# Kernel optimization log

Hardware: AMD Instinct MI355X
Metric: run time of the kernel (lower is better)

## Reference

```python
import jax, jax.numpy as jnp
import numpy as np

N = 50000      # nodes
E = 800000     # edges (avg degree 16)
DIM = 256      # in_channels == heads * out_channels
H = 8          # heads
C = DIM // H   # per-head out_channels = 32
EDGE_DIM = 2
NEG_SLOPE = 0.2


def setup_inputs() -> dict:
    key = jax.random.key(0)
    ks = jax.random.split(key, 8)
    x = jax.random.normal(ks[0], (N, DIM), dtype=jnp.float32)
    edge_index = jax.random.randint(ks[1], (2, E), 0, N, dtype=jnp.int32)
    edge_attr = jax.random.normal(ks[2], (E, EDGE_DIM), dtype=jnp.float32)
    s = 1.0 / np.sqrt(DIM)
    W_l = jax.random.normal(ks[3], (DIM, H * C), dtype=jnp.float32) * s   # lin_l (src)
    W_r = jax.random.normal(ks[4], (DIM, H * C), dtype=jnp.float32) * s   # lin_r (dst)
    W_e = jax.random.normal(ks[5], (EDGE_DIM, H * C), dtype=jnp.float32) * (1.0 / np.sqrt(EDGE_DIM))
    att = jax.random.normal(ks[6], (H, C), dtype=jnp.float32) * s         # attention vector a
    bias = jnp.zeros((H * C,), dtype=jnp.float32)
    return {"x": x, "edge_index": edge_index, "edge_attr": edge_attr,
            "W_l": W_l, "W_r": W_r, "W_e": W_e, "att": att, "bias": bias}


def reference(x, edge_index, edge_attr, W_l, W_r, W_e, att, bias):
    src, dst = edge_index[0], edge_index[1]
    # --- add self loops; fill_value='mean' => scatter-mean of incoming edge_attr per node ---
    attr_sum = jax.ops.segment_sum(edge_attr, dst, num_segments=N)          # [N, 2]
    cnt = jax.ops.segment_sum(jnp.ones((edge_attr.shape[0], 1), edge_attr.dtype), dst, num_segments=N)
    loop_attr = attr_sum / jnp.maximum(cnt, 1.0)                             # [N, 2], 0 for isolated nodes
    idx = jnp.arange(N, dtype=src.dtype)
    src_a = jnp.concatenate([src, idx])                                      # [E+N]
    dst_a = jnp.concatenate([dst, idx])
    ea = jnp.concatenate([edge_attr, loop_attr], axis=0)                     # [E+N, 2]
    # --- GATv2: project src/dst/edge features ---
    x_l = (x @ W_l).reshape(N, H, C)
    x_r = (x @ W_r).reshape(N, H, C)
    e_e = (ea @ W_e).reshape(-1, H, C)                                       # [E+N, H, C]
    m = x_l[src_a] + x_r[dst_a] + e_e                                        # [E+N, H, C]
    score = jnp.einsum('ehc,hc->eh', jax.nn.leaky_relu(m, NEG_SLOPE), att)   # [E+N, H]
    # --- segment softmax over incoming edges of each dst (self loop guarantees >=1 edge) ---
    smax = jax.ops.segment_max(score, dst_a, num_segments=N)                 # [N, H]
    ex = jnp.exp(score - smax[dst_a])
    denom = jax.ops.segment_sum(ex, dst_a, num_segments=N)                   # [N, H]
    alpha = ex / denom[dst_a]                                                # [E+N, H]
    # --- weighted scatter-add of src messages ---
    out = jax.ops.segment_sum(alpha[..., None] * x_l[src_a], dst_a, num_segments=N)  # [N, H, C]
    return out.reshape(N, H * C) + bias
```

## Files before the change

kernel.cpp:

```cpp
#include <hip/hip_runtime.h>
#include <hip/hip_bf16.h>

#define NN 50000
#define NPAD 53248
#define EE 800000
#define DIM 256
#define NEG_SLOPE 0.2f
#define LOG2E 1.44269504088896f

#define GEMM_BLOCKS 1564
#define FILL_BLOCKS 3125
#define MIX_BLOCKS  15625
#define WT_BLOCKS   512

typedef __attribute__((ext_vector_type(8))) short short8;
typedef __attribute__((ext_vector_type(4))) float f32x4;
typedef __attribute__((ext_vector_type(2))) float v2f;

__device__ __forceinline__ unsigned short f2bf(float f) {
    unsigned u = __float_as_uint(f);
    unsigned r = (u + 0x7fffu + ((u >> 16) & 1u)) >> 16;
    return (unsigned short)r;
}
__device__ __forceinline__ float u2f_lo(unsigned u) {
    return __uint_as_float(u << 16);
}
__device__ __forceinline__ float u2f_hi(unsigned u) {
    return __uint_as_float(u & 0xffff0000u);
}

__device__ __forceinline__ float red8(float s) {
    int t;
    t = __builtin_amdgcn_update_dpp(0, __float_as_int(s), 0xB1, 0xF, 0xF, true);
    s += __int_as_float(t);
    t = __builtin_amdgcn_update_dpp(0, __float_as_int(s), 0x4E, 0xF, 0xF, true);
    s += __int_as_float(t);
    t = __builtin_amdgcn_update_dpp(0, __float_as_int(s), 0x141, 0xF, 0xF, true);
    s += __int_as_float(t);
    return s;
}

__global__ __launch_bounds__(256) void k_prep_count(
    const float* __restrict__ x, const float* __restrict__ Wl,
    const float* __restrict__ Wr, const int* __restrict__ ei,
    unsigned short* __restrict__ xb, unsigned short* __restrict__ wt,
    int* __restrict__ cnt, int* __restrict__ rank)
{
    int b = blockIdx.x;
    if (b < MIX_BLOCKS) {
        int g = b / 5;
        if (b - g * 5 == 0) {
            int e = g * 256 + threadIdx.x;
            int dst = ei[EE + e];
            rank[e] = atomicAdd(&cnt[dst], 1);
        } else {
            int ci = b - g - 1;
            int i = (ci * 256 + threadIdx.x) * 4;
            float4 v = *(const float4*)(x + i);
            ushort4 o;
            o.x = f2bf(v.x); o.y = f2bf(v.y); o.z = f2bf(v.z); o.w = f2bf(v.w);
            *(ushort4*)(xb + i) = o;
        }
    } else {
        int idx = (b - MIX_BLOCKS) * 256 + threadIdx.x;
        int n = idx >> 8, k = idx & 255;
        float v = (n < 256) ? Wl[k * 256 + n] : Wr[k * 256 + (n - 256)];
        wt[idx] = f2bf(v);
    }
}

__global__ __launch_bounds__(1024) void k_scan(
    const int* __restrict__ cnt, int* __restrict__ row_start)
{
    __shared__ int wsum[16];
    int tid = threadIdx.x, lane = tid & 63, wid = tid >> 6;
    int4 v[13];
#pragma unroll
    for (int p = 0; p < 13; ++p)
        v[p] = *(const int4*)(cnt + p * 4096 + tid * 4);
    int carry = 0;
#pragma unroll
    for (int p = 0; p < 13; ++p) {
        int4 vv = v[p];
        int tsum = vv.x + vv.y + vv.z + vv.w;
        int s = tsum;
#pragma unroll
        for (int off = 1; off < 64; off <<= 1) {
            int t = __shfl_up(s, off, 64);
            if (lane >= off) s += t;
        }
        if (lane == 63) wsum[wid] = s;
        __syncthreads();
        int wpre = 0, tot = 0;
#pragma unroll
        for (int w = 0; w < 16; ++w) {
            int xv = wsum[w];
            tot += xv;
            if (w < wid) wpre += xv;
        }
        int ex = carry + wpre + (s - tsum);
        int4 o;
        o.x = ex;
        o.y = o.x + vv.x;
        o.z = o.y + vv.y;
        o.w = o.z + vv.z;
        *(int4*)(row_start + p * 4096 + tid * 4) = o;
        carry += tot;
        __syncthreads();
    }
}

__global__ __launch_bounds__(256) void k_gemm_fill(
    const unsigned short* __restrict__ xb, const unsigned short* __restrict__ wt,
    const int* __restrict__ ei, const float* __restrict__ ea,
    const int* __restrict__ row_start, const int* __restrict__ rank,
    unsigned short* __restrict__ xl, unsigned short* __restrict__ xr,
    uint2* __restrict__ edge_rec)
{
    __shared__ short sAB[8192];
    int tid = threadIdx.x;

    if (blockIdx.x >= GEMM_BLOCKS) {
        int e = (blockIdx.x - GEMM_BLOCKS) * 256 + tid;
        if (e < EE) {
            int src = ei[e];
            int dst = ei[EE + e];
            float2 a = *(const float2*)(ea + 2 * e);
            int pos = row_start[dst] + rank[e];
            unsigned packed = ((unsigned)f2bf(a.y) << 16) | f2bf(a.x);
            edge_rec[pos] = make_uint2((unsigned)src, packed);
        }
        return;
    }

    int bid = blockIdx.x;
    const int q = GEMM_BLOCKS / 8, r = GEMM_BLOCKS % 8;
    int xcd = bid & 7, kk = bid >> 3;
    int wg = (xcd < r) ? xcd * (q + 1) + kk
                       : r * (q + 1) + (xcd - r) * q + kk;

    int wid = tid >> 6, lane = tid & 63;
    int mt = wg >> 2, nt = wg & 3;
    int mBase = mt * 128, nBase = nt * 128;
    int wm = (wid & 1) * 64, wn = (wid >> 1) * 64;
    int qq4 = lane >> 4, mh = lane & 15;

    f32x4 acc[4][4];
#pragma unroll
    for (int i = 0; i < 4; ++i)
#pragma unroll
        for (int j = 0; j < 4; ++j)
            acc[i][j] = (f32x4){0.f, 0.f, 0.f, 0.f};

    int aoff[4], boff[4];
#pragma unroll
    for (int f = 0; f < 4; ++f) {
        int rr = wm + f * 16 + mh;
        aoff[f] = (rr * 4 + (qq4 ^ (rr & 3))) * 8;
        int nl = wn + f * 16 + mh;
        boff[f] = 4096 + (nl * 4 + (qq4 ^ (nl & 3))) * 8;
    }

    for (int k0 = 0; k0 < 256; k0 += 32) {
        __syncthreads();
#pragma unroll
        for (int it = 0; it < 4; ++it) {
            int L = it * 256 + tid;
            const unsigned short* g;
            if (L < 512) {
                int rr = L >> 2;
                int q2 = (L & 3) ^ (rr & 3);
                int grow = mBase + rr;
                if (grow > NN - 1) grow = NN - 1;
                g = xb + (size_t)grow * 256 + k0 + q2 * 8;
            } else {
                int LB = L - 512;
                int nl = LB >> 2;
                int q2 = (LB & 3) ^ (nl & 3);
                g = wt + (size_t)(nBase + nl) * 256 + k0 + q2 * 8;
            }
            short* lp = sAB + (it * 256 + wid * 64) * 8;
            __builtin_amdgcn_global_load_lds(
                (const __attribute__((address_space(1))) void*)g,
                (__attribute__((address_space(3))) void*)lp, 16, 0, 0);
        }
        __syncthreads();

        short8 af[4], bfr[4];
#pragma unroll
        for (int f = 0; f < 4; ++f) af[f]  = *(const short8*)(sAB + aoff[f]);
#pragma unroll
        for (int f = 0; f < 4; ++f) bfr[f] = *(const short8*)(sAB + boff[f]);
#pragma unroll
        for (int i = 0; i < 4; ++i)
#pragma unroll
            for (int j = 0; j < 4; ++j)
                acc[i][j] = __builtin_amdgcn_mfma_f32_16x16x32_bf16(
                    af[i], bfr[j], acc[i][j], 0, 0, 0);
    }

    unsigned short* cb = (nt < 2) ? xl : xr;
    int chalf = (nt & 1) * 128;
#pragma unroll
    for (int i = 0; i < 4; ++i)
#pragma unroll
        for (int j = 0; j < 4; ++j)
#pragma unroll
            for (int rr = 0; rr < 4; ++rr) {
                int row = mBase + wm + i * 16 + qq4 * 4 + rr;
                if (row < NN) {
                    int col = chalf + wn + j * 16 + mh;
                    cb[(size_t)row * 256 + col] = f2bf(acc[i][j][rr]);
                }
            }
}

__global__ __launch_bounds__(256) void k_attn(
    const unsigned short* __restrict__ xl, const unsigned short* __restrict__ xr,
    const int* __restrict__ row_start, const uint2* __restrict__ edge_rec,
    const float* __restrict__ W_e, const float* __restrict__ att,
    const float* __restrict__ bias, float* __restrict__ out)
{
    int n = __builtin_amdgcn_readfirstlane(blockIdx.x * 4 + (threadIdx.x >> 6));
    if (n >= NN) return;
    int lane = threadIdx.x & 63;
    int j = lane * 4;

    uint2 xru = *(const uint2*)(xr + ((size_t)n << 8) + j);
    v2f xr01 = {u2f_lo(xru.x), u2f_hi(xru.x)};
    v2f xr23 = {u2f_lo(xru.y), u2f_hi(xru.y)};
    float4 av = *(const float4*)(att + j);
    v2f att01 = {av.x * LOG2E, av.y * LOG2E};
    v2f att23 = {av.z * LOG2E, av.w * LOG2E};
    float4 w0v = *(const float4*)(W_e + j);
    float4 w1v = *(const float4*)(W_e + 256 + j);
    v2f we0_01 = {w0v.x, w0v.y}, we0_23 = {w0v.z, w0v.w};
    v2f we1_01 = {w1v.x, w1v.y}, we1_23 = {w1v.z, w1v.w};
    const v2f sl2 = {NEG_SLOPE, NEG_SLOPE};

    int rs = __builtin_amdgcn_readfirstlane(row_start[n]);
    int cn = __builtin_amdgcn_readfirstlane(row_start[n + 1]) - rs;

    float D = 0.0f, la0 = 0.0f, la1 = 0.0f;
    v2f acc01 = {0.f, 0.f}, acc23 = {0.f, 0.f};

    auto body = [&](uint2 ru, float a0, float a1) {
        v2f xl01 = {u2f_lo(ru.x), u2f_hi(ru.x)};
        v2f xl23 = {u2f_lo(ru.y), u2f_hi(ru.y)};
        v2f a0v = {a0, a0}, a1v = {a1, a1};
        v2f m01 = xl01 + xr01;
        v2f m23 = xl23 + xr23;
        m01 = __builtin_elementwise_fma(a0v, we0_01, m01);
        m23 = __builtin_elementwise_fma(a0v, we0_23, m23);
        m01 = __builtin_elementwise_fma(a1v, we1_01, m01);
        m23 = __builtin_elementwise_fma(a1v, we1_23, m23);
        v2f t01 = __builtin_elementwise_max(m01, m01 * sl2);
        v2f t23 = __builtin_elementwise_max(m23, m23 * sl2);
        v2f sv = t01 * att01;
        sv = __builtin_elementwise_fma(t23, att23, sv);
        float s = sv.x + sv.y;
        s = red8(s);
        float w = __builtin_amdgcn_exp2f(s);
        D += w;
        v2f wv = {w, w};
        acc01 = __builtin_elementwise_fma(wv, xl01, acc01);
        acc23 = __builtin_elementwise_fma(wv, xl23, acc23);
    };

    int done = 0;
    while (done < cn) {
        int m = cn - done; if (m > 64) m = 64;
        int ridx = rs + done + lane;
        if (ridx > EE + 63) ridx = EE + 63;
        uint2 rc = edge_rec[ridx];
        int rcx = (int)rc.x, rca = (int)rc.y;

        auto gat = [&](int k) -> uint2 {
            unsigned sidx = (unsigned)__builtin_amdgcn_readlane(rcx, k);
            return *(const uint2*)(xl + ((size_t)sidx << 8) + j);
        };
        auto proc = [&](uint2 xu, int k) {
            unsigned pk = (unsigned)__builtin_amdgcn_readlane(rca, k);
            float a0 = __uint_as_float(pk << 16);
            float a1 = __uint_as_float(pk & 0xffff0000u);
            la0 += a0; la1 += a1;
            body(xu, a0, a1);
        };

        uint2 x0 = gat(0), x1 = gat(1), x2 = gat(2), x3 = gat(3);
        uint2 x4 = gat(4), x5 = gat(5), x6 = gat(6), x7 = gat(7);
        for (int i = 0; i < m; i += 8) {
            proc(x0, i);
            if (i +  8 < m) x0 = gat(i +  8);
            if (i + 1 < m) { proc(x1, i + 1); if (i +  9 < m) x1 = gat(i +  9); }
            if (i + 2 < m) { proc(x2, i + 2); if (i + 10 < m) x2 = gat(i + 10); }
            if (i + 3 < m) { proc(x3, i + 3); if (i + 11 < m) x3 = gat(i + 11); }
            if (i + 4 < m) { proc(x4, i + 4); if (i + 12 < m) x4 = gat(i + 12); }
            if (i + 5 < m) { proc(x5, i + 5); if (i + 13 < m) x5 = gat(i + 13); }
            if (i + 6 < m) { proc(x6, i + 6); if (i + 14 < m) x6 = gat(i + 14); }
            if (i + 7 < m) { proc(x7, i + 7); if (i + 15 < m) x7 = gat(i + 15); }
        }
        done += m;
    }

    float invc = 1.0f / fmaxf((float)cn, 1.0f);
    uint2 xs = *(const uint2*)(xl + ((size_t)n << 8) + j);
    body(xs, la0 * invc, la1 * invc);

    float invD = 1.0f / D;
    float4 b4 = *(const float4*)(bias + j);
    float4 o;
    o.x = fmaf(acc01.x, invD, b4.x);
    o.y = fmaf(acc01.y, invD, b4.y);
    o.z = fmaf(acc23.x, invD, b4.z);
    o.w = fmaf(acc23.y, invD, b4.w);
    *(float4*)(out + (size_t)n * 256 + j) = o;
}

extern "C" void kernel_launch(void* const* d_in, const int* in_sizes, int n_in,
                              void* d_out, int out_size, void* d_ws, size_t ws_size,
                              hipStream_t stream)
{
    const float* x    = (const float*)d_in[0];
    const int*   ei   = (const int*)  d_in[1];
    const float* ea   = (const float*)d_in[2];
    const float* Wl   = (const float*)d_in[3];
    const float* Wr   = (const float*)d_in[4];
    const float* We   = (const float*)d_in[5];
    const float* att  = (const float*)d_in[6];
    const float* bias = (const float*)d_in[7];
    float* out = (float*)d_out;

    char* ws = (char*)d_ws;
    size_t off = 0;
    unsigned short* xl = (unsigned short*)(ws + off); off += (size_t)NN * 256 * 2;
    unsigned short* xr = (unsigned short*)(ws + off); off += (size_t)NN * 256 * 2;
    unsigned short* xb = (unsigned short*)(ws + off); off += (size_t)NN * 256 * 2;
    uint2*  edge_rec   = (uint2*)(ws + off);          off += (size_t)(EE + 64) * 8;
    int*    cnt        = (int*)(ws + off);            off += (size_t)NPAD * 4;
    int*    row_st     = (int*)(ws + off);            off += (size_t)NPAD * 4;
    int*    rank       = (int*)(ws + off);            off += (size_t)EE * 4;
    unsigned short* wt = (unsigned short*)(ws + off); off += (size_t)512 * 256 * 2;

    hipMemsetAsync(edge_rec + EE, 0, 64 * sizeof(uint2) + NPAD * sizeof(int), stream);

    k_prep_count<<<MIX_BLOCKS + WT_BLOCKS, 256, 0, stream>>>(
        x, Wl, Wr, ei, xb, wt, cnt, rank);
    k_scan      <<<1, 1024, 0, stream>>>(cnt, row_st);
    k_gemm_fill <<<GEMM_BLOCKS + FILL_BLOCKS, 256, 0, stream>>>(
        xb, wt, ei, ea, row_st, rank, xl, xr, edge_rec);
    k_attn      <<<12500, 256, 0, stream>>>(
        xl, xr, row_st, edge_rec, We, att, bias, out);
}
```

Baseline: 258.7 us.

## Partition degree-count atomics per XCD and store compact 16-bit ranks

Replaces the single global per-node counter with eight per-XCD counter arrays. Each edge does a workgroup-scope atomic on the array for its own XCC (read from a hardware register) and records a 16-bit rank that packs the XCD id with a local rank. A new pre-reduction kernel turns the per-XCD counts into exclusive offsets and writes per-node totals, which the existing scan then scans in place. The aim is to avoid contended device-scope atomics across XCDs and to halve the rank traffic. The cost is an extra kernel launch, a larger counter buffer to clear and read, and reliance on workgroup-scope atomics staying coherent within an XCD's L2.

```diff
diff --git a/kernel.cpp b/kernel.cpp
--- a/kernel.cpp
+++ b/kernel.cpp
@@ -7,11 +7,13 @@
 #define DIM 256
 #define NEG_SLOPE 0.2f
 #define LOG2E 1.44269504088896f
+#define CSTR 50048
 
 #define GEMM_BLOCKS 1564
 #define FILL_BLOCKS 3125
 #define MIX_BLOCKS  15625
 #define WT_BLOCKS   512
+#define PRERED_BLOCKS 208
 
 typedef __attribute__((ext_vector_type(8))) short short8;
 typedef __attribute__((ext_vector_type(4))) float f32x4;
@@ -44,7 +46,7 @@
     const float* __restrict__ x, const float* __restrict__ Wl,
     const float* __restrict__ Wr, const int* __restrict__ ei,
     unsigned short* __restrict__ xb, unsigned short* __restrict__ wt,
-    int* __restrict__ cnt, int* __restrict__ rank)
+    unsigned* __restrict__ cnt_x, unsigned short* __restrict__ rank16)
 {
     int b = blockIdx.x;
     if (b < MIX_BLOCKS) {
@@ -52,7 +54,13 @@
         if (b - g * 5 == 0) {
             int e = g * 256 + threadIdx.x;
             int dst = ei[EE + e];
-            rank[e] = atomicAdd(&cnt[dst], 1);
+            unsigned xcc;
+            asm volatile("s_getreg_b32 %0, hwreg(HW_REG_XCC_ID)" : "=s"(xcc));
+            xcc &= 7u;
+            unsigned rl = __hip_atomic_fetch_add(
+                &cnt_x[xcc * CSTR + (unsigned)dst], 1u,
+                __ATOMIC_RELAXED, __HIP_MEMORY_SCOPE_WORKGROUP);
+            rank16[e] = (unsigned short)((xcc << 8) | rl);
         } else {
             int ci = b - g - 1;
             int i = (ci * 256 + threadIdx.x) * 4;
@@ -69,15 +77,30 @@
     }
 }
 
-__global__ __launch_bounds__(1024) void k_scan(
-    const int* __restrict__ cnt, int* __restrict__ row_start)
+__global__ __launch_bounds__(256) void k_prered(
+    unsigned* __restrict__ cnt_x, int* __restrict__ row_st)
+{
+    int d = blockIdx.x * 256 + threadIdx.x;
+    unsigned s = 0;
+    if (d < CSTR) {
+#pragma unroll
+        for (int c = 0; c < 8; ++c) {
+            unsigned v = cnt_x[c * CSTR + d];
+            cnt_x[c * CSTR + d] = s;
+            s += v;
+        }
+    }
+    row_st[d] = (int)s;
+}
+
+__global__ __launch_bounds__(1024) void k_scan(int* __restrict__ a)
 {
     __shared__ int wsum[16];
     int tid = threadIdx.x, lane = tid & 63, wid = tid >> 6;
     int4 v[13];
 #pragma unroll
     for (int p = 0; p < 13; ++p)
-        v[p] = *(const int4*)(cnt + p * 4096 + tid * 4);
+        v[p] = *(const int4*)(a + p * 4096 + tid * 4);
     int carry = 0;
 #pragma unroll
     for (int p = 0; p < 13; ++p) {
@@ -104,7 +127,7 @@
         o.y = o.x + vv.x;
         o.z = o.y + vv.y;
         o.w = o.z + vv.z;
-        *(int4*)(row_start + p * 4096 + tid * 4) = o;
+        *(int4*)(a + p * 4096 + tid * 4) = o;
         carry += tot;
         __syncthreads();
     }
@@ -113,7 +136,8 @@
 __global__ __launch_bounds__(256) void k_gemm_fill(
     const unsigned short* __restrict__ xb, const unsigned short* __restrict__ wt,
     const int* __restrict__ ei, const float* __restrict__ ea,
-    const int* __restrict__ row_start, const int* __restrict__ rank,
+    const int* __restrict__ row_start, const unsigned short* __restrict__ rank16,
+    const unsigned* __restrict__ cnt_x,
     unsigned short* __restrict__ xl, unsigned short* __restrict__ xr,
     uint2* __restrict__ edge_rec)
 {
@@ -126,7 +150,9 @@
             int src = ei[e];
             int dst = ei[EE + e];
             float2 a = *(const float2*)(ea + 2 * e);
-            int pos = row_start[dst] + rank[e];
+            int rk = rank16[e];
+            int c = rk >> 8, rl = rk & 255;
+            int pos = row_start[dst] + (int)cnt_x[c * CSTR + dst] + rl;
             unsigned packed = ((unsigned)f2bf(a.y) << 16) | f2bf(a.x);
             edge_rec[pos] = make_uint2((unsigned)src, packed);
         }
@@ -337,18 +363,20 @@
     unsigned short* xr = (unsigned short*)(ws + off); off += (size_t)NN * 256 * 2;
     unsigned short* xb = (unsigned short*)(ws + off); off += (size_t)NN * 256 * 2;
     uint2*  edge_rec   = (uint2*)(ws + off);          off += (size_t)(EE + 64) * 8;
-    int*    cnt        = (int*)(ws + off);            off += (size_t)NPAD * 4;
+    unsigned* cnt_x    = (unsigned*)(ws + off);       off += (size_t)8 * CSTR * 4;
     int*    row_st     = (int*)(ws + off);            off += (size_t)NPAD * 4;
-    int*    rank       = (int*)(ws + off);            off += (size_t)EE * 4;
+    unsigned short* rank16 = (unsigned short*)(ws + off); off += (size_t)EE * 2;
     unsigned short* wt = (unsigned short*)(ws + off); off += (size_t)512 * 256 * 2;
 
-    hipMemsetAsync(edge_rec + EE, 0, 64 * sizeof(uint2) + NPAD * sizeof(int), stream);
+    hipMemsetAsync(edge_rec + EE, 0,
+                   64 * sizeof(uint2) + (size_t)8 * CSTR * 4, stream);
 
     k_prep_count<<<MIX_BLOCKS + WT_BLOCKS, 256, 0, stream>>>(
-        x, Wl, Wr, ei, xb, wt, cnt, rank);
-    k_scan      <<<1, 1024, 0, stream>>>(cnt, row_st);
+        x, Wl, Wr, ei, xb, wt, cnt_x, rank16);
+    k_prered    <<<PRERED_BLOCKS, 256, 0, stream>>>(cnt_x, row_st);
+    k_scan      <<<1, 1024, 0, stream>>>(row_st);
     k_gemm_fill <<<GEMM_BLOCKS + FILL_BLOCKS, 256, 0, stream>>>(
-        xb, wt, ei, ea, row_st, rank, xl, xr, edge_rec);
+        xb, wt, ei, ea, row_st, rank16, cnt_x, xl, xr, edge_rec);
     k_attn      <<<12500, 256, 0, stream>>>(
         xl, xr, row_st, edge_rec, We, att, bias, out);
 }
```

After: 262.7 us. Within noise of the previous version (+1.5%).

## Replace global-atomic CSR build with per-block LDS histograms and column scan

Applied to the files above, without the earlier changes.

Builds the destination-sorted edge list with per-block shared-memory histograms (16-bit packed counters) instead of global atomics per edge. A column scan over the block histograms and a global scan give each block a deterministic offset, and a fill kernel recomputes local ranks with LDS atomics. This removes the per-edge rank array and the contended global atomics. In exchange it adds more kernel launches, reuses the bf16 x buffer as histogram scratch after the GEMM, and serialises the GEMM with the CSR build instead of running them in one fused launch.

```diff
diff --git a/kernel.cpp b/kernel.cpp
--- a/kernel.cpp
+++ b/kernel.cpp
@@ -8,10 +8,14 @@
 #define NEG_SLOPE 0.2f
 #define LOG2E 1.44269504088896f
 
+#define CSTR 50000
+#define HIST_BLOCKS 256
+#define EPB 3125
+
 #define GEMM_BLOCKS 1564
-#define FILL_BLOCKS 3125
-#define MIX_BLOCKS  15625
+#define CVT_BLOCKS  12500
 #define WT_BLOCKS   512
+#define COLS_BLOCKS 208
 
 typedef __attribute__((ext_vector_type(8))) short short8;
 typedef __attribute__((ext_vector_type(4))) float f32x4;
@@ -40,98 +44,32 @@
     return s;
 }
 
-__global__ __launch_bounds__(256) void k_prep_count(
+__global__ __launch_bounds__(256) void k_prep(
     const float* __restrict__ x, const float* __restrict__ Wl,
-    const float* __restrict__ Wr, const int* __restrict__ ei,
-    unsigned short* __restrict__ xb, unsigned short* __restrict__ wt,
-    int* __restrict__ cnt, int* __restrict__ rank)
+    const float* __restrict__ Wr,
+    unsigned short* __restrict__ xb, unsigned short* __restrict__ wt)
 {
     int b = blockIdx.x;
-    if (b < MIX_BLOCKS) {
-        int g = b / 5;
-        if (b - g * 5 == 0) {
-            int e = g * 256 + threadIdx.x;
-            int dst = ei[EE + e];
-            rank[e] = atomicAdd(&cnt[dst], 1);
-        } else {
-            int ci = b - g - 1;
-            int i = (ci * 256 + threadIdx.x) * 4;
-            float4 v = *(const float4*)(x + i);
-            ushort4 o;
-            o.x = f2bf(v.x); o.y = f2bf(v.y); o.z = f2bf(v.z); o.w = f2bf(v.w);
-            *(ushort4*)(xb + i) = o;
-        }
+    if (b < CVT_BLOCKS) {
+        int i = (b * 256 + threadIdx.x) * 4;
+        float4 v = *(const float4*)(x + i);
+        ushort4 o;
+        o.x = f2bf(v.x); o.y = f2bf(v.y); o.z = f2bf(v.z); o.w = f2bf(v.w);
+        *(ushort4*)(xb + i) = o;
     } else {
-        int idx = (b - MIX_BLOCKS) * 256 + threadIdx.x;
+        int idx = (b - CVT_BLOCKS) * 256 + threadIdx.x;
         int n = idx >> 8, k = idx & 255;
         float v = (n < 256) ? Wl[k * 256 + n] : Wr[k * 256 + (n - 256)];
         wt[idx] = f2bf(v);
     }
 }
 
-__global__ __launch_bounds__(1024) void k_scan(
-    const int* __restrict__ cnt, int* __restrict__ row_start)
-{
-    __shared__ int wsum[16];
-    int tid = threadIdx.x, lane = tid & 63, wid = tid >> 6;
-    int4 v[13];
-#pragma unroll
-    for (int p = 0; p < 13; ++p)
-        v[p] = *(const int4*)(cnt + p * 4096 + tid * 4);
-    int carry = 0;
-#pragma unroll
-    for (int p = 0; p < 13; ++p) {
-        int4 vv = v[p];
-        int tsum = vv.x + vv.y + vv.z + vv.w;
-        int s = tsum;
-#pragma unroll
-        for (int off = 1; off < 64; off <<= 1) {
-            int t = __shfl_up(s, off, 64);
-            if (lane >= off) s += t;
-        }
-        if (lane == 63) wsum[wid] = s;
-        __syncthreads();
-        int wpre = 0, tot = 0;
-#pragma unroll
-        for (int w = 0; w < 16; ++w) {
-            int xv = wsum[w];
-            tot += xv;
-            if (w < wid) wpre += xv;
-        }
-        int ex = carry + wpre + (s - tsum);
-        int4 o;
-        o.x = ex;
-        o.y = o.x + vv.x;
-        o.z = o.y + vv.y;
-        o.w = o.z + vv.z;
-        *(int4*)(row_start + p * 4096 + tid * 4) = o;
-        carry += tot;
-        __syncthreads();
-    }
-}
-
-__global__ __launch_bounds__(256) void k_gemm_fill(
+__global__ __launch_bounds__(256) void k_gemm(
     const unsigned short* __restrict__ xb, const unsigned short* __restrict__ wt,
-    const int* __restrict__ ei, const float* __restrict__ ea,
-    const int* __restrict__ row_start, const int* __restrict__ rank,
-    unsigned short* __restrict__ xl, unsigned short* __restrict__ xr,
-    uint2* __restrict__ edge_rec)
+    unsigned short* __restrict__ xl, unsigned short* __restrict__ xr)
 {
     __shared__ short sAB[8192];
     int tid = threadIdx.x;
-
-    if (blockIdx.x >= GEMM_BLOCKS) {
-        int e = (blockIdx.x - GEMM_BLOCKS) * 256 + tid;
-        if (e < EE) {
-            int src = ei[e];
-            int dst = ei[EE + e];
-            float2 a = *(const float2*)(ea + 2 * e);
-            int pos = row_start[dst] + rank[e];
-            unsigned packed = ((unsigned)f2bf(a.y) << 16) | f2bf(a.x);
-            edge_rec[pos] = make_uint2((unsigned)src, packed);
-        }
-        return;
-    }
 
     int bid = blockIdx.x;
     const int q = GEMM_BLOCKS / 8, r = GEMM_BLOCKS % 8;
@@ -213,6 +151,118 @@
                     cb[(size_t)row * 256 + col] = f2bf(acc[i][j][rr]);
                 }
             }
+}
+
+__global__ __launch_bounds__(512) void k_hist(
+    const int* __restrict__ ei, unsigned short* __restrict__ ghist)
+{
+    __shared__ unsigned lh[CSTR / 2];
+    int tid = threadIdx.x, blk = blockIdx.x;
+    for (int i = tid; i < CSTR / 2; i += 512) lh[i] = 0u;
+    __syncthreads();
+    int base = blk * EPB;
+#pragma unroll
+    for (int it = 0; it < 7; ++it) {
+        int idx = it * 512 + tid;
+        if (idx < EPB) {
+            int dst = ei[EE + base + idx];
+            atomicAdd(&lh[dst >> 1], 1u << ((dst & 1) * 16));
+        }
+    }
+    __syncthreads();
+    unsigned* gout = (unsigned*)(ghist + (size_t)blk * CSTR);
+    for (int i = tid; i < CSTR / 2; i += 512) gout[i] = lh[i];
+}
+
+__global__ __launch_bounds__(256) void k_colscan(
+    unsigned short* __restrict__ ghist, int* __restrict__ row_st,
+    uint2* __restrict__ edge_rec)
+{
+    int d = blockIdx.x * 256 + threadIdx.x;
+    if (blockIdx.x == 0 && threadIdx.x < 128)
+        ((unsigned*)(edge_rec + EE))[threadIdx.x] = 0u;
+    if (d < CSTR) {
+        unsigned s = 0;
+#pragma unroll 8
+        for (int b = 0; b < HIST_BLOCKS; ++b) {
+            size_t o = (size_t)b * CSTR + d;
+            unsigned v = ghist[o];
+            ghist[o] = (unsigned short)s;
+            s += v;
+        }
+        row_st[d] = (int)s;
+    } else {
+        row_st[d] = 0;
+    }
+}
+
+__global__ __launch_bounds__(1024) void k_scan(int* __restrict__ a)
+{
+    __shared__ int wsum[16];
+    int tid = threadIdx.x, lane = tid & 63, wid = tid >> 6;
+    int4 v[13];
+#pragma unroll
+    for (int p = 0; p < 13; ++p)
+        v[p] = *(const int4*)(a + p * 4096 + tid * 4);
+    int carry = 0;
+#pragma unroll
+    for (int p = 0; p < 13; ++p) {
+        int4 vv = v[p];
+        int tsum = vv.x + vv.y + vv.z + vv.w;
+        int s = tsum;
+#pragma unroll
+        for (int off = 1; off < 64; off <<= 1) {
+            int t = __shfl_up(s, off, 64);
+            if (lane >= off) s += t;
+        }
+        if (lane == 63) wsum[wid] = s;
+        __syncthreads();
+        int wpre = 0, tot = 0;
+#pragma unroll
+        for (int w = 0; w < 16; ++w) {
+            int xv = wsum[w];
+            tot += xv;
+            if (w < wid) wpre += xv;
+        }
+        int ex = carry + wpre + (s - tsum);
+        int4 o;
+        o.x = ex;
+        o.y = o.x + vv.x;
+        o.z = o.y + vv.y;
+        o.w = o.z + vv.z;
+        *(int4*)(a + p * 4096 + tid * 4) = o;
+        carry += tot;
+        __syncthreads();
+    }
+}
+
+__global__ __launch_bounds__(512) void k_fill(
+    const int* __restrict__ ei, const float* __restrict__ ea,
+    const int* __restrict__ row_start, const unsigned short* __restrict__ ghist,
+    uint2* __restrict__ edge_rec)
+{
+    __shared__ unsigned lh[CSTR / 2];
+    int tid = threadIdx.x, blk = blockIdx.x;
+    for (int i = tid; i < CSTR / 2; i += 512) lh[i] = 0u;
+    __syncthreads();
+    int base = blk * EPB;
+    const unsigned short* gh = ghist + (size_t)blk * CSTR;
+#pragma unroll
+    for (int it = 0; it < 7; ++it) {
+        int idx = it * 512 + tid;
+        if (idx < EPB) {
+            int e = base + idx;
+            int src = ei[e];
+            int dst = ei[EE + e];
+            float2 a = *(const float2*)(ea + 2 * e);
+            unsigned sh = (dst & 1) * 16;
+            unsigned old = atomicAdd(&lh[dst >> 1], 1u << sh);
+            int rl = (int)((old >> sh) & 0xffffu);
+            int pos = row_start[dst] + (int)gh[dst] + rl;
+            unsigned packed = ((unsigned)f2bf(a.y) << 16) | f2bf(a.x);
+            edge_rec[pos] = make_uint2((unsigned)src, packed);
+        }
+    }
 }
 
 __global__ __launch_bounds__(256) void k_attn(
@@ -337,18 +387,16 @@
     unsigned short* xr = (unsigned short*)(ws + off); off += (size_t)NN * 256 * 2;
     unsigned short* xb = (unsigned short*)(ws + off); off += (size_t)NN * 256 * 2;
     uint2*  edge_rec   = (uint2*)(ws + off);          off += (size_t)(EE + 64) * 8;
-    int*    cnt        = (int*)(ws + off);            off += (size_t)NPAD * 4;
     int*    row_st     = (int*)(ws + off);            off += (size_t)NPAD * 4;
-    int*    rank       = (int*)(ws + off);            off += (size_t)EE * 4;
     unsigned short* wt = (unsigned short*)(ws + off); off += (size_t)512 * 256 * 2;
-
-    hipMemsetAsync(edge_rec + EE, 0, 64 * sizeof(uint2) + NPAD * sizeof(int), stream);
-
-    k_prep_count<<<MIX_BLOCKS + WT_BLOCKS, 256, 0, stream>>>(
-        x, Wl, Wr, ei, xb, wt, cnt, rank);
-    k_scan      <<<1, 1024, 0, stream>>>(cnt, row_st);
-    k_gemm_fill <<<GEMM_BLOCKS + FILL_BLOCKS, 256, 0, stream>>>(
-        xb, wt, ei, ea, row_st, rank, xl, xr, edge_rec);
-    k_attn      <<<12500, 256, 0, stream>>>(
+    unsigned short* ghist = xb;
+
+    k_prep    <<<CVT_BLOCKS + WT_BLOCKS, 256, 0, stream>>>(x, Wl, Wr, xb, wt);
+    k_gemm    <<<GEMM_BLOCKS, 256, 0, stream>>>(xb, wt, xl, xr);
+    k_hist    <<<HIST_BLOCKS, 512, 0, stream>>>(ei, ghist);
+    k_colscan <<<COLS_BLOCKS, 256, 0, stream>>>(ghist, row_st, edge_rec);
+    k_scan    <<<1, 1024, 0, stream>>>(row_st);
+    k_fill    <<<HIST_BLOCKS, 512, 0, stream>>>(ei, ea, row_st, ghist, edge_rec);
+    k_attn    <<<12500, 256, 0, stream>>>(
         xl, xr, row_st, edge_rec, We, att, bias, out);
 }
```

Result: slower. 277.7 us (+7.3%).
